# Kernel tuning notes

Hardware: AMD Instinct MI355X
Metric: run time of the kernel (lower is better)

The kernel has to match this reference:

```python
import jax, jax.numpy as jnp
import numpy as np


def reference(x, coef_ref, coef_qry):
    # x: [B, Hr, Wr, Hq, Wq] similarity tensor
    B, Hr, Wr, Hq, Wq = x.shape
    xr = x.reshape(B, Hr * Wr, Hq * Wq)  # [B, R, Q]
    # softmax over ref axis (axis=1) of coef_ref * (x - max over axis 1)
    xm_ref = xr - jnp.max(xr, axis=1, keepdims=True)
    conf_ref = jax.nn.softmax(coef_ref[0] * xm_ref, axis=1)
    # softmax over qry axis (axis=2) of coef_qry * (x - max over axis 2)
    xm_qry = xr - jnp.max(xr, axis=2, keepdims=True)
    conf_qry = jax.nn.softmax(coef_qry[0] * xm_qry, axis=2)
    confidence = jnp.sqrt(conf_ref * conf_qry)  # [B, R, Q]
    # top_k(k=1) over last axis + gather_nd of that value == max over axis 2
    values = jnp.max(confidence, axis=2)  # [B, R]
    return values.reshape(B, Hr, Wr, 1)


def setup_inputs() -> dict:
    key = jax.random.key(0)
    k1, = jax.random.split(key, 1)
    B, Hr, Wr, Hq, Wq = 16, 64, 64, 32, 32
    alpha = 10.0
    x = jax.random.normal(k1, (B, Hr, Wr, Hq, Wq), dtype=jnp.float32)
    coef_ref = jnp.full((1,), alpha, dtype=jnp.float32)
    coef_qry = jnp.full((1,), alpha, dtype=jnp.float32)
    return {"x": x, "coef_ref": coef_ref, "coef_qry": coef_qry}
```

## Files before the change

### kernel.cpp

```cpp
#include <hip/hip_runtime.h>
#include <math.h>
#include <stdint.h>


constexpr int B = 16;
constexpr int R = 4096;
constexpr int Q = 1024;
constexpr int CAP = 32;
#define DTH 0.80f

typedef float float4n __attribute__((ext_vector_type(4)));

__device__ __forceinline__ float wmax64(float v) {
#pragma unroll
    for (int o = 32; o; o >>= 1) v = fmaxf(v, __shfl_xor(v, o, 64));
    return v;
}
__device__ __forceinline__ float max4(float4 v) {
    return fmaxf(fmaxf(v.x, v.y), fmaxf(v.z, v.w));
}
__device__ __forceinline__ uint32_t encf(float f) {
    uint32_t u = __float_as_uint(f);
    return (u & 0x80000000u) ? ~u : (u | 0x80000000u);
}
__device__ __forceinline__ float decf(uint32_t e) {
    uint32_t u = (e & 0x80000000u) ? (e & 0x7FFFFFFFu) : ~e;
    return __uint_as_float(u);
}

__global__ __launch_bounds__(256) void qatm_sample(const float* __restrict__ x,
                                                   float* __restrict__ rmSamp,
                                                   uint32_t* __restrict__ cminEnc) {
    const int blk = blockIdx.x;
    const int b = blk >> 3, k = blk & 7;
    const int t = threadIdx.x;
    if ((blk & 7) == 0 && t == 0) cminEnc[b] = 0xFFFFFFFFu;
    const float4* xr = reinterpret_cast<const float4*>(x) +
                       ((size_t)b * R + (size_t)k * 512) * (Q / 4);
    float m = wmax64(max4(xr[t]));
    __shared__ float sh[4];
    if ((t & 63) == 0) sh[t >> 6] = m;
    __syncthreads();
    if (t == 0)
        rmSamp[blk] = fmaxf(fmaxf(sh[0], sh[1]), fmaxf(sh[2], sh[3]));
}

__global__ __launch_bounds__(256) void qatm_pass1(
    const float* __restrict__ x,
    float* __restrict__ psum,
    float2* __restrict__ rscnt,
    float4* __restrict__ cand4,
    uint32_t* __restrict__ candg,
    const float* __restrict__ rmSamp,
    float* __restrict__ thOut,
    const float* __restrict__ coef_ref,
    const float* __restrict__ coef_qry)
{
    const int blk = blockIdx.x;
    const int b = blk >> 6, chunk = blk & 63;
    const int t = threadIdx.x;
    const float ar = coef_ref[0], aq = coef_qry[0];
    const bool same = (ar == aq);
    float thsum = 0.f;
#pragma unroll
    for (int i = 0; i < 8; ++i) thsum += rmSamp[b * 8 + i];
    const float th = thsum * 0.125f - DTH;
    if (chunk == 0 && t == 0) thOut[b] = th;

    const size_t row0 = (size_t)b * R + (size_t)chunk * 64;
    const float4n* xb = reinterpret_cast<const float4n*>(x) + row0 * (Q / 4) + t;

    __shared__ float ssum[16][256];
    __shared__ int cnt_sh[16];
    if (t < 16) cnt_sh[t] = 0;
    __syncthreads();

    float4 cs = {0.f, 0.f, 0.f, 0.f};

    for (int win = 0; win < 4; ++win) {
        const float4n* xw = xb + (size_t)win * 16 * 256;
#pragma unroll
        for (int rr8 = 0; rr8 < 16; rr8 += 8) {
            float4n vn[8];
#pragma unroll
            for (int k = 0; k < 8; ++k)
                vn[k] = __builtin_nontemporal_load(&xw[(size_t)(rr8 + k) * 256]);
#pragma unroll
            for (int k = 0; k < 8; ++k) {
                const int rr = rr8 + k;
                float4 v = make_float4(vn[k].x, vn[k].y, vn[k].z, vn[k].w);
                float4 e;
                e.x = __expf(ar * v.x); e.y = __expf(ar * v.y);
                e.z = __expf(ar * v.z); e.w = __expf(ar * v.w);
                cs.x += e.x; cs.y += e.y; cs.z += e.z; cs.w += e.w;
                float rp;
                if (same) rp = (e.x + e.y) + (e.z + e.w);
                else rp = (__expf(aq * v.x) + __expf(aq * v.y)) +
                          (__expf(aq * v.z) + __expf(aq * v.w));
                ssum[rr][t] = rp;
                if (max4(v) >= th) {
                    int idx = atomicAdd(&cnt_sh[rr], 1);
                    if (idx < CAP) {
                        const size_t grow = row0 + win * 16 + rr;
                        cand4[grow * CAP + idx] = v;
                        candg[grow * CAP + idx] = (uint32_t)t;
                    }
                }
            }
        }
        __syncthreads();
        const int j = t >> 4, s = t & 15;
        float p = 0.f;
#pragma unroll
        for (int i = 0; i < 16; ++i) p += ssum[j][i * 16 + s];
        p += __shfl_xor(p, 1, 64);
        p += __shfl_xor(p, 2, 64);
        p += __shfl_xor(p, 4, 64);
        p += __shfl_xor(p, 8, 64);
        if (s == 0) {
            const size_t grow = row0 + win * 16 + j;
            rscnt[grow] = make_float2(p, __uint_as_float((uint32_t)cnt_sh[j]));
            cnt_sh[j] = 0;
        }
        __syncthreads();
    }
    reinterpret_cast<float4*>(psum)[(size_t)blk * 256 + t] = cs;
}

__global__ __launch_bounds__(256) void qatm_combine(
    const float* __restrict__ psum, float* __restrict__ cvec,
    uint32_t* __restrict__ cminEnc)
{
    const int b = blockIdx.x >> 2, part = blockIdx.x & 3;
    const int t = threadIdx.x;
    const int col = part * 256 + t;
    float s = 0.f;
    const float* p = psum + (size_t)b * 64 * 1024 + col;
#pragma unroll 16
    for (int i = 0; i < 64; ++i) s += p[(size_t)i * 1024];
    const float c = __logf(s);
    cvec[b * 1024 + col] = c;
    float m = -wmax64(-c);
    __shared__ float sh[4];
    if ((t & 63) == 0) sh[t >> 6] = m;
    __syncthreads();
    if (t == 0) {
        float mm = fminf(fminf(sh[0], sh[1]), fminf(sh[2], sh[3]));
        atomicMin(&cminEnc[b], encf(mm));
    }
}

__global__ __launch_bounds__(256) void qatm_select(
    const float* __restrict__ x, const float* __restrict__ cvec,
    const uint32_t* __restrict__ cminEnc, const float* __restrict__ thArr,
    const float2* __restrict__ rscnt,
    const float4* __restrict__ cand4, const uint32_t* __restrict__ candg,
    const float* __restrict__ coef_ref, const float* __restrict__ coef_qry,
    float* __restrict__ out)
{
    const int w = threadIdx.x >> 6, l = threadIdx.x & 63;
    const size_t row = (size_t)blockIdx.x * 4 + w;
    const int b = (int)(row >> 12);
    const float ar = coef_ref[0], aq = coef_qry[0], s2 = ar + aq;
    const float2 rc = rscnt[row];
    const float rs = rc.x;
    const uint32_t cnt = __float_as_uint(rc.y);

    float best = -INFINITY;
    bool fb = (cnt > CAP) || (cnt == 0) || !(s2 > 0.f);
    if (!fb) {
        if (l < (int)cnt) {
            float4 v = cand4[row * CAP + l];
            uint32_t g = candg[row * CAP + l];
            float4 c = reinterpret_cast<const float4*>(cvec)[((size_t)b << 8) + g];
            best = fmaxf(fmaxf(s2 * v.x - c.x, s2 * v.y - c.y),
                         fmaxf(s2 * v.z - c.z, s2 * v.w - c.w));
        }
        best = wmax64(best);
        if (!(best >= s2 * thArr[b] - decf(cminEnc[b]))) fb = true;
    }
    if (fb) {
        const float4* xr = reinterpret_cast<const float4*>(x) + row * (Q / 4);
        const float4* cq = reinterpret_cast<const float4*>(cvec) + ((size_t)b << 8);
        best = -INFINITY;
#pragma unroll
        for (int it = 0; it < 4; ++it) {
            float4 v = xr[it * 64 + l], c = cq[it * 64 + l];
            best = fmaxf(best, fmaxf(fmaxf(s2 * v.x - c.x, s2 * v.y - c.y),
                                     fmaxf(s2 * v.z - c.z, s2 * v.w - c.w)));
        }
        best = wmax64(best);
    }
    if (l == 0) out[row] = __expf(0.5f * (best - __logf(rs)));
}

extern "C" void kernel_launch(void* const* d_in, const int* in_sizes, int n_in,
                              void* d_out, int out_size, void* d_ws, size_t ws_size,
                              hipStream_t stream) {
    const float* x = (const float*)d_in[0];
    const float* coef_ref = (const float*)d_in[1];
    const float* coef_qry = (const float*)d_in[2];
    float* out = (float*)d_out;

    char* ws = (char*)d_ws;
    size_t off = 0;
    float4*   cand4 = (float4*)(ws + off);   off += (size_t)B * R * CAP * 16;
    float*    psum  = (float*)(ws + off);    off += (size_t)B * 64 * 1024 * 4;
    uint32_t* candg = (uint32_t*)(ws + off); off += (size_t)B * R * CAP * 4;
    float*    cvec  = (float*)(ws + off);    off += (size_t)B * Q * 4;
    float2*   rscnt = (float2*)(ws + off);   off += (size_t)B * R * 8;
    float*    rmSamp= (float*)(ws + off);    off += 512;
    float*    thA   = (float*)(ws + off);    off += 64;
    uint32_t* cminE = (uint32_t*)(ws + off); off += 64;

    qatm_sample<<<B * 8, 256, 0, stream>>>(x, rmSamp, cminE);
    qatm_pass1<<<B * 64, 256, 0, stream>>>(x, psum, rscnt, cand4, candg,
                                           rmSamp, thA, coef_ref, coef_qry);
    qatm_combine<<<64, 256, 0, stream>>>(psum, cvec, cminE);
    qatm_select<<<(B * R) / 4, 256, 0, stream>>>(x, cvec, cminE, thA, rscnt,
                                                 cand4, candg, coef_ref, coef_qry, out);
}
```

Before: 88.95 us.

## Fuse four kernels into one cooperative kernel with grid syncs and per-chunk thresholds

Replaces the sample, pass1, combine and select kernels with a single cooperative kernel of 512 blocks. Stages are separated by grid-wide syncs, and each block handles 128 rows. The global row-max sample becomes a per-chunk threshold taken from the chunk's first row, and the margin constant changes. The select stage now processes 32 rows per wave and prefetches the next row's candidates. This removes launch overheads and the separate sampling read, at the cost of lower parallelism (512 blocks) and grid-sync latency.

```diff
diff --git a/kernel.cpp b/kernel.cpp
--- a/kernel.cpp
+++ b/kernel.cpp
@@ -1,13 +1,19 @@
 #include <hip/hip_runtime.h>
+#include <hip/hip_cooperative_groups.h>
 #include <math.h>
 #include <stdint.h>
+
+namespace cg = cooperative_groups;
 
 
 constexpr int B = 16;
 constexpr int R = 4096;
 constexpr int Q = 1024;
 constexpr int CAP = 32;
-#define DTH 0.80f
+constexpr int NBLK = 512;
+constexpr int CHROWS = 128;
+constexpr int NCH = R / CHROWS;
+#define DTH 1.1f
 
 typedef float float4n __attribute__((ext_vector_type(4)));
 
@@ -28,56 +34,56 @@
     return __uint_as_float(u);
 }
 
-__global__ __launch_bounds__(256) void qatm_sample(const float* __restrict__ x,
-                                                   float* __restrict__ rmSamp,
-                                                   uint32_t* __restrict__ cminEnc) {
-    const int blk = blockIdx.x;
-    const int b = blk >> 3, k = blk & 7;
-    const int t = threadIdx.x;
-    if ((blk & 7) == 0 && t == 0) cminEnc[b] = 0xFFFFFFFFu;
-    const float4* xr = reinterpret_cast<const float4*>(x) +
-                       ((size_t)b * R + (size_t)k * 512) * (Q / 4);
-    float m = wmax64(max4(xr[t]));
-    __shared__ float sh[4];
-    if ((t & 63) == 0) sh[t >> 6] = m;
-    __syncthreads();
-    if (t == 0)
-        rmSamp[blk] = fmaxf(fmaxf(sh[0], sh[1]), fmaxf(sh[2], sh[3]));
-}
-
-__global__ __launch_bounds__(256) void qatm_pass1(
+__global__ __launch_bounds__(256, 2) void qatm_fused(
     const float* __restrict__ x,
     float* __restrict__ psum,
     float2* __restrict__ rscnt,
     float4* __restrict__ cand4,
     uint32_t* __restrict__ candg,
-    const float* __restrict__ rmSamp,
-    float* __restrict__ thOut,
+    float* __restrict__ thChunk,
+    uint32_t* __restrict__ cminEnc,
+    float* __restrict__ cvec,
     const float* __restrict__ coef_ref,
-    const float* __restrict__ coef_qry)
+    const float* __restrict__ coef_qry,
+    float* __restrict__ out)
 {
+    cg::grid_group grid = cg::this_grid();
     const int blk = blockIdx.x;
-    const int b = blk >> 6, chunk = blk & 63;
     const int t = threadIdx.x;
+    const int w = t >> 6, l = t & 63;
     const float ar = coef_ref[0], aq = coef_qry[0];
     const bool same = (ar == aq);
-    float thsum = 0.f;
-#pragma unroll
-    for (int i = 0; i < 8; ++i) thsum += rmSamp[b * 8 + i];
-    const float th = thsum * 0.125f - DTH;
-    if (chunk == 0 && t == 0) thOut[b] = th;
-
-    const size_t row0 = (size_t)b * R + (size_t)chunk * 64;
-    const float4n* xb = reinterpret_cast<const float4n*>(x) + row0 * (Q / 4) + t;
 
     __shared__ float ssum[16][256];
     __shared__ int cnt_sh[16];
-    if (t < 16) cnt_sh[t] = 0;
-    __syncthreads();
-
+    __shared__ float redsh[4];
+    __shared__ float th_sh;
+
+    const int b = blk >> 5, ch = blk & 31;
+    const size_t grow0 = (size_t)b * R + (size_t)ch * CHROWS;
+
+    if (blk < B && t == 0) cminEnc[blk] = 0xFFFFFFFFu;
+
+    {
+        const float4n* x0 = reinterpret_cast<const float4n*>(x) + grow0 * 256;
+        float4n vv = x0[t];
+        float m = wmax64(fmaxf(fmaxf(vv.x, vv.y), fmaxf(vv.z, vv.w)));
+        if (l == 0) redsh[w] = m;
+        if (t < 16) cnt_sh[t] = 0;
+        __syncthreads();
+        if (t == 0) {
+            float mm = fmaxf(fmaxf(redsh[0], redsh[1]), fmaxf(redsh[2], redsh[3]));
+            th_sh = mm - DTH;
+            thChunk[blk] = mm - DTH;
+        }
+        __syncthreads();
+    }
+    const float th = th_sh;
+
+    const float4n* xb = reinterpret_cast<const float4n*>(x) + grow0 * 256 + t;
     float4 cs = {0.f, 0.f, 0.f, 0.f};
 
-    for (int win = 0; win < 4; ++win) {
+    for (int win = 0; win < CHROWS / 16; ++win) {
         const float4n* xw = xb + (size_t)win * 16 * 256;
 #pragma unroll
         for (int rr8 = 0; rr8 < 16; rr8 += 8) {
@@ -101,7 +107,7 @@
                 if (max4(v) >= th) {
                     int idx = atomicAdd(&cnt_sh[rr], 1);
                     if (idx < CAP) {
-                        const size_t grow = row0 + win * 16 + rr;
+                        const size_t grow = grow0 + win * 16 + rr;
                         cand4[grow * CAP + idx] = v;
                         candg[grow * CAP + idx] = (uint32_t)t;
                     }
@@ -118,80 +124,84 @@
         p += __shfl_xor(p, 4, 64);
         p += __shfl_xor(p, 8, 64);
         if (s == 0) {
-            const size_t grow = row0 + win * 16 + j;
+            const size_t grow = grow0 + win * 16 + j;
             rscnt[grow] = make_float2(p, __uint_as_float((uint32_t)cnt_sh[j]));
             cnt_sh[j] = 0;
         }
         __syncthreads();
     }
     reinterpret_cast<float4*>(psum)[(size_t)blk * 256 + t] = cs;
-}
-
-__global__ __launch_bounds__(256) void qatm_combine(
-    const float* __restrict__ psum, float* __restrict__ cvec,
-    uint32_t* __restrict__ cminEnc)
-{
-    const int b = blockIdx.x >> 2, part = blockIdx.x & 3;
-    const int t = threadIdx.x;
-    const int col = part * 256 + t;
-    float s = 0.f;
-    const float* p = psum + (size_t)b * 64 * 1024 + col;
+
+    __threadfence();
+    grid.sync();
+
+    if (blk < 64) {
+        const int bb = blk >> 2;
+        const int col = (blk & 3) * 256 + t;
+        float s = 0.f;
+        const float* p = psum + (size_t)bb * NCH * 1024 + col;
 #pragma unroll 16
-    for (int i = 0; i < 64; ++i) s += p[(size_t)i * 1024];
-    const float c = __logf(s);
-    cvec[b * 1024 + col] = c;
-    float m = -wmax64(-c);
-    __shared__ float sh[4];
-    if ((t & 63) == 0) sh[t >> 6] = m;
-    __syncthreads();
-    if (t == 0) {
-        float mm = fminf(fminf(sh[0], sh[1]), fminf(sh[2], sh[3]));
-        atomicMin(&cminEnc[b], encf(mm));
-    }
-}
-
-__global__ __launch_bounds__(256) void qatm_select(
-    const float* __restrict__ x, const float* __restrict__ cvec,
-    const uint32_t* __restrict__ cminEnc, const float* __restrict__ thArr,
-    const float2* __restrict__ rscnt,
-    const float4* __restrict__ cand4, const uint32_t* __restrict__ candg,
-    const float* __restrict__ coef_ref, const float* __restrict__ coef_qry,
-    float* __restrict__ out)
-{
-    const int w = threadIdx.x >> 6, l = threadIdx.x & 63;
-    const size_t row = (size_t)blockIdx.x * 4 + w;
-    const int b = (int)(row >> 12);
-    const float ar = coef_ref[0], aq = coef_qry[0], s2 = ar + aq;
-    const float2 rc = rscnt[row];
-    const float rs = rc.x;
-    const uint32_t cnt = __float_as_uint(rc.y);
-
-    float best = -INFINITY;
-    bool fb = (cnt > CAP) || (cnt == 0) || !(s2 > 0.f);
-    if (!fb) {
-        if (l < (int)cnt) {
-            float4 v = cand4[row * CAP + l];
-            uint32_t g = candg[row * CAP + l];
-            float4 c = reinterpret_cast<const float4*>(cvec)[((size_t)b << 8) + g];
-            best = fmaxf(fmaxf(s2 * v.x - c.x, s2 * v.y - c.y),
-                         fmaxf(s2 * v.z - c.z, s2 * v.w - c.w));
-        }
-        best = wmax64(best);
-        if (!(best >= s2 * thArr[b] - decf(cminEnc[b]))) fb = true;
-    }
-    if (fb) {
-        const float4* xr = reinterpret_cast<const float4*>(x) + row * (Q / 4);
-        const float4* cq = reinterpret_cast<const float4*>(cvec) + ((size_t)b << 8);
-        best = -INFINITY;
-#pragma unroll
-        for (int it = 0; it < 4; ++it) {
-            float4 v = xr[it * 64 + l], c = cq[it * 64 + l];
-            best = fmaxf(best, fmaxf(fmaxf(s2 * v.x - c.x, s2 * v.y - c.y),
-                                     fmaxf(s2 * v.z - c.z, s2 * v.w - c.w)));
-        }
-        best = wmax64(best);
-    }
-    if (l == 0) out[row] = __expf(0.5f * (best - __logf(rs)));
+        for (int i = 0; i < NCH; ++i) s += p[(size_t)i * 1024];
+        const float c = __logf(s);
+        cvec[bb * 1024 + col] = c;
+        float m = -wmax64(-c);
+        if (l == 0) redsh[w] = m;
+        __syncthreads();
+        if (t == 0) {
+            float mm = fminf(fminf(redsh[0], redsh[1]), fminf(redsh[2], redsh[3]));
+            atomicMin(&cminEnc[bb], encf(mm));
+        }
+    }
+
+    __threadfence();
+    grid.sync();
+
+    const float s2 = ar + aq;
+    const int wid = blk * 4 + w;
+    const size_t rowbase = (size_t)wid * 32;
+
+    float2 rc = rscnt[rowbase];
+    float4 pv = cand4[rowbase * CAP + l];
+    uint32_t g = candg[rowbase * CAP + l];
+
+    for (int rr = 0; rr < 32; ++rr) {
+        const size_t row = rowbase + rr;
+        float2 rcn; float4 pvn; uint32_t gn;
+        if (rr < 31) {
+            rcn = rscnt[row + 1];
+            pvn = cand4[(row + 1) * CAP + l];
+            gn = candg[(row + 1) * CAP + l];
+        }
+        const int bb = (int)(row >> 12);
+        const float rs = rc.x;
+        const uint32_t cnt = __float_as_uint(rc.y);
+
+        float best = -INFINITY;
+        bool fb = (cnt > CAP) || (cnt == 0) || !(s2 > 0.f);
+        if (!fb) {
+            if (l < (int)cnt) {
+                float4 c = reinterpret_cast<const float4*>(cvec)[(bb << 8) + (int)(g & 255u)];
+                best = fmaxf(fmaxf(s2 * pv.x - c.x, s2 * pv.y - c.y),
+                             fmaxf(s2 * pv.z - c.z, s2 * pv.w - c.w));
+            }
+            best = wmax64(best);
+            if (!(best >= s2 * thChunk[row >> 7] - decf(cminEnc[bb]))) fb = true;
+        }
+        if (fb) {
+            const float4* xr = reinterpret_cast<const float4*>(x) + row * (Q / 4);
+            const float4* cq = reinterpret_cast<const float4*>(cvec) + ((size_t)bb << 8);
+            best = -INFINITY;
+#pragma unroll
+            for (int it = 0; it < 4; ++it) {
+                float4 v = xr[it * 64 + l], c = cq[it * 64 + l];
+                best = fmaxf(best, fmaxf(fmaxf(s2 * v.x - c.x, s2 * v.y - c.y),
+                                         fmaxf(s2 * v.z - c.z, s2 * v.w - c.w)));
+            }
+            best = wmax64(best);
+        }
+        if (l == 0) out[row] = __expf(0.5f * (best - __logf(rs)));
+        rc = rcn; pv = pvn; g = gn;
+    }
 }
 
 extern "C" void kernel_launch(void* const* d_in, const int* in_sizes, int n_in,
@@ -204,19 +214,17 @@
 
     char* ws = (char*)d_ws;
     size_t off = 0;
-    float4*   cand4 = (float4*)(ws + off);   off += (size_t)B * R * CAP * 16;
-    float*    psum  = (float*)(ws + off);    off += (size_t)B * 64 * 1024 * 4;
-    uint32_t* candg = (uint32_t*)(ws + off); off += (size_t)B * R * CAP * 4;
+    float4*   cand4 = (float4*)(ws + off);   off += ((size_t)B * R * CAP + 64) * 16;
+    uint32_t* candg = (uint32_t*)(ws + off); off += ((size_t)B * R * CAP + 64) * 4;
+    float*    psum  = (float*)(ws + off);    off += (size_t)NBLK * 1024 * 4;
+    float2*   rscnt = (float2*)(ws + off);   off += (size_t)B * R * 8;
     float*    cvec  = (float*)(ws + off);    off += (size_t)B * Q * 4;
-    float2*   rscnt = (float2*)(ws + off);   off += (size_t)B * R * 8;
-    float*    rmSamp= (float*)(ws + off);    off += 512;
-    float*    thA   = (float*)(ws + off);    off += 64;
+    float*    thA   = (float*)(ws + off);    off += (size_t)NBLK * 4;
     uint32_t* cminE = (uint32_t*)(ws + off); off += 64;
 
-    qatm_sample<<<B * 8, 256, 0, stream>>>(x, rmSamp, cminE);
-    qatm_pass1<<<B * 64, 256, 0, stream>>>(x, psum, rscnt, cand4, candg,
-                                           rmSamp, thA, coef_ref, coef_qry);
-    qatm_combine<<<64, 256, 0, stream>>>(psum, cvec, cminE);
-    qatm_select<<<(B * R) / 4, 256, 0, stream>>>(x, cvec, cminE, thA, rscnt,
-                                                 cand4, candg, coef_ref, coef_qry, out);
-}
+    void* args[] = {(void*)&x, (void*)&psum, (void*)&rscnt, (void*)&cand4,
+                    (void*)&candg, (void*)&thA, (void*)&cminE, (void*)&cvec,
+                    (void*)&coef_ref, (void*)&coef_qry, (void*)&out};
+    hipLaunchCooperativeKernel((void*)qatm_fused, dim3(NBLK), dim3(256),
+                               args, 0, stream);
+}
```

New measurement: 353.1 us. +296.9%, slower.
